# Optimization experiments

Measured on AMD Instinct MI355X. Metric: run time of the kernel, lower is better.

Reference implementation:

```python
import jax, jax.numpy as jnp
import numpy as np

HIDDEN = 1024
HEADS = 16
HEAD_DIM = HIDDEN // HEADS
B, S = 2, 2048


def setup_inputs() -> dict:
    key = jax.random.key(0)
    ks = jax.random.split(key, 9)
    sc = 1.0 / np.sqrt(HIDDEN)
    return {
        "hidden_state": jax.random.normal(ks[0], (B, S, HIDDEN), dtype=jnp.float32),
        "wq": jax.random.normal(ks[1], (HIDDEN, HIDDEN), dtype=jnp.float32) * sc,
        "bq": jax.random.normal(ks[2], (HIDDEN,), dtype=jnp.float32) * 0.01,
        "wk": jax.random.normal(ks[3], (HIDDEN, HIDDEN), dtype=jnp.float32) * sc,
        "bk": jax.random.normal(ks[4], (HIDDEN,), dtype=jnp.float32) * 0.01,
        "wv": jax.random.normal(ks[5], (HIDDEN, HIDDEN), dtype=jnp.float32) * sc,
        "bv": jax.random.normal(ks[6], (HIDDEN,), dtype=jnp.float32) * 0.01,
        "wo": jax.random.normal(ks[7], (HIDDEN, HIDDEN), dtype=jnp.float32) * sc,
        "bo": jax.random.normal(ks[8], (HIDDEN,), dtype=jnp.float32) * 0.01,
    }


def reference(hidden_state, wq, bq, wk, bk, wv, bv, wo, bo):
    b, s, _ = hidden_state.shape

    def split_head(x):  # [B,S,H*D] -> [B,H,S,D]
        return x.reshape(b, s, HEADS, HEAD_DIM).transpose(0, 2, 1, 3)

    q = split_head(hidden_state @ wq + bq)
    k = split_head(hidden_state @ wk + bk)
    v = split_head(hidden_state @ wv + bv)

    # NOTE: original scales by sqrt(hidden_size), NOT sqrt(head_dim)
    scale = 1.0 / jnp.sqrt(jnp.float32(HIDDEN))
    scores = jnp.einsum("bhqd,bhkd->bhqk", q, k) * scale  # [B,H,S,S]
    probs = jax.nn.softmax(scores, axis=-1)
    out = jnp.einsum("bhqk,bhkd->bhqd", probs, v)  # [B,H,S,D]

    # Faithful to source: transpose(-1,-2) then view (this is the original's
    # layout, which differs from the conventional transpose(1,2) merge)
    out = out.transpose(0, 1, 3, 2).reshape(b, -1, HEADS * HEAD_DIM)
    return out @ wo + bo
```

## Files before the change

### kernel.cpp

```cpp
#include <hip/hip_runtime.h>
#include <stdint.h>


typedef unsigned short u16;
typedef __bf16 bf16x8 __attribute__((ext_vector_type(8)));
typedef u16 u16x8 __attribute__((ext_vector_type(8)));
typedef u16 u16x4 __attribute__((ext_vector_type(4)));
typedef float f32x4 __attribute__((ext_vector_type(4)));

#define DEV static __device__ __forceinline__

DEV bf16x8 as_bf16x8(u16x8 u) { union { u16x8 u; bf16x8 b; } c; c.u = u; return c.b; }
DEV u16 f2bf(float f) {
  uint32_t u = __float_as_uint(f);
  u += 0x7fffu + ((u >> 16) & 1u);
  return (u16)(u >> 16);
}
DEV uint32_t pk_rhu(float a, float b) {
  uint32_t ua = (__float_as_uint(a) + 0x8000u) >> 16;
  uint32_t ub = (__float_as_uint(b) + 0x8000u) & 0xffff0000u;
  return ua | ub;
}

DEV void gll16(const u16* g, u16* lds) {
  __builtin_amdgcn_global_load_lds((const __attribute__((address_space(1))) void*)g,
                                   (__attribute__((address_space(3))) void*)lds,
                                   16, 0, 0);
}

__global__ __launch_bounds__(256) void prep_kernel(
    const float* __restrict__ hid, const float* __restrict__ w0,
    const float* __restrict__ w1, const float* __restrict__ w2,
    const float* __restrict__ w3, u16* __restrict__ Ah,
    u16* __restrict__ Wt) {
  __shared__ __align__(16) float T[64][68];
  int bid = blockIdx.x, t = threadIdx.x;
  if (bid < 2048) {
    int i = (bid * 256 + t) * 8;
    f32x4 a = *(const f32x4*)&hid[i];
    f32x4 b = *(const f32x4*)&hid[i + 4];
    u16x8 o;
#pragma unroll
    for (int j = 0; j < 4; ++j) { o[j] = f2bf(a[j]); o[j + 4] = f2bf(b[j]); }
    *(u16x8*)&Ah[i] = o;
    return;
  }
  int tb = bid - 2048;
  int z = tb >> 8, rem = tb & 255;
  const float* W = (z == 0) ? w0 : (z == 1) ? w1 : (z == 2) ? w2 : w3;
  u16* O = Wt + (size_t)z * 1024 * 1024;
  int r0 = (rem >> 4) * 64, c0 = (rem & 15) * 64;
  int i = t >> 2, js = (t & 3) * 16;
#pragma unroll
  for (int jj = 0; jj < 16; jj += 4)
    *(f32x4*)&T[i][js + jj] = *(const f32x4*)&W[(size_t)(r0 + i) * 1024 + c0 + js + jj];
  __syncthreads();
#pragma unroll
  for (int seg = 0; seg < 2; ++seg) {
    u16x8 v;
#pragma unroll
    for (int jj = 0; jj < 8; ++jj) v[jj] = f2bf(T[js + seg * 8 + jj][i]);
    *(u16x8*)&O[(size_t)(c0 + i) * 1024 + r0 + js + seg * 8] = v;
  }
}

DEV void gemm_body(const u16* __restrict__ A, const u16* __restrict__ Bt,
                   const float* __restrict__ bias, u16* __restrict__ C,
                   int mode, float scale) {
  __shared__ __align__(16) u16 As[128 * 32], Bs[128 * 32];
  int tid = threadIdx.x, lane = tid & 63, w = tid >> 6;
  int quad = lane >> 4, l15 = lane & 15;
  int m0 = blockIdx.x * 128, n0 = blockIdx.y * 128;
  int wm = w >> 1, wn = w & 1;
  f32x4 acc[4][4] = {};

  for (int k0 = 0; k0 < 1024; k0 += 32) {
    __syncthreads();
#pragma unroll
    for (int i = 0; i < 2; ++i) {
      int idx = i * 256 + w * 64 + lane;
      int row = idx >> 2, cs = idx & 3, c = cs ^ ((row >> 1) & 3);
      gll16(A + (size_t)(m0 + row) * 1024 + k0 + c * 8, &As[(i * 256 + w * 64) * 8]);
      gll16(Bt + (size_t)(n0 + row) * 1024 + k0 + c * 8, &Bs[(i * 256 + w * 64) * 8]);
    }
    __syncthreads();
    bf16x8 af[4], bfr[4];
#pragma unroll
    for (int mt = 0; mt < 4; ++mt) {
      int row = wm * 64 + mt * 16 + l15;
      af[mt] = as_bf16x8(*(const u16x8*)&As[row * 32 + (quad ^ ((row >> 1) & 3)) * 8]);
    }
#pragma unroll
    for (int nt = 0; nt < 4; ++nt) {
      int row = wn * 64 + nt * 16 + l15;
      bfr[nt] = as_bf16x8(*(const u16x8*)&Bs[row * 32 + (quad ^ ((row >> 1) & 3)) * 8]);
    }
#pragma unroll
    for (int mt = 0; mt < 4; ++mt)
#pragma unroll
      for (int nt = 0; nt < 4; ++nt)
        acc[mt][nt] = __builtin_amdgcn_mfma_f32_16x16x32_bf16(af[mt], bfr[nt], acc[mt][nt], 0, 0, 0);
  }

#pragma unroll
  for (int nt = 0; nt < 4; ++nt) {
    int n = n0 + wn * 64 + nt * 16 + l15;
    float bv = bias[n];
#pragma unroll
    for (int mt = 0; mt < 4; ++mt) {
      int mbase = m0 + wm * 64 + mt * 16 + quad * 4;
      if (mode == 2) {
        int b = mbase >> 11, s = mbase & 2047, h = n >> 6, d = n & 63;
        size_t base = (((size_t)(b * 16 + h)) * 64 + d) * 2048 + s;
        u16x4 pk;
#pragma unroll
        for (int r = 0; r < 4; ++r) pk[r] = f2bf((acc[mt][nt][r] + bv) * scale);
        *(u16x4*)&C[base] = pk;
      } else {
#pragma unroll
        for (int r = 0; r < 4; ++r) {
          int m = mbase + r;
          int b = m >> 11, s = m & 2047, h = n >> 6, d = n & 63;
          C[(((size_t)(b * 16 + h)) * 2048 + s) * 64 + d] =
              f2bf((acc[mt][nt][r] + bv) * scale);
        }
      }
    }
  }
}

__global__ __launch_bounds__(256) void qkv_gemm(
    const u16* __restrict__ A, const u16* __restrict__ Wt,
    const float* __restrict__ bq, const float* __restrict__ bk,
    const float* __restrict__ bv, u16* __restrict__ Qb, u16* __restrict__ Kb,
    u16* __restrict__ Vt) {
  int z = blockIdx.z;
  const u16* Bt = Wt + (size_t)z * 1024 * 1024;
  const float* bias = (z == 0) ? bq : (z == 1) ? bk : bv;
  u16* C = (z == 0) ? Qb : (z == 1) ? Kb : Vt;
  gemm_body(A, Bt, bias, C, (z == 2) ? 2 : 1, (z == 0) ? 0.03125f : 1.0f);
}

__global__ __launch_bounds__(256) void out_gemm(
    const u16* __restrict__ A, const u16* __restrict__ Wt,
    const float* __restrict__ bo, float* __restrict__ C) {
  const u16* Bt = Wt + (size_t)3 * 1024 * 1024;
  __shared__ __align__(16) u16 As[64 * 32], Bs[128 * 32];
  int tid = threadIdx.x, lane = tid & 63, w = tid >> 6;
  int quad = lane >> 4, l15 = lane & 15;
  int m0 = blockIdx.x * 64, n0 = blockIdx.y * 128;
  f32x4 acc[4][2] = {};

  for (int k0 = 0; k0 < 1024; k0 += 32) {
    __syncthreads();
    {
      int idx = w * 64 + lane;
      int row = idx >> 2, cs = idx & 3, c = cs ^ ((row >> 1) & 3);
      gll16(A + (size_t)(m0 + row) * 1024 + k0 + c * 8, &As[(w * 64) * 8]);
#pragma unroll
      for (int i = 0; i < 2; ++i) {
        int bidx = i * 256 + w * 64 + lane;
        int brow = bidx >> 2, bcs = bidx & 3, bc = bcs ^ ((brow >> 1) & 3);
        gll16(Bt + (size_t)(n0 + brow) * 1024 + k0 + bc * 8,
              &Bs[(i * 256 + w * 64) * 8]);
      }
    }
    __syncthreads();
    bf16x8 af[4], bfr[2];
#pragma unroll
    for (int mt = 0; mt < 4; ++mt) {
      int row = mt * 16 + l15;
      af[mt] = as_bf16x8(*(const u16x8*)&As[row * 32 + (quad ^ ((row >> 1) & 3)) * 8]);
    }
#pragma unroll
    for (int nt = 0; nt < 2; ++nt) {
      int row = w * 32 + nt * 16 + l15;
      bfr[nt] = as_bf16x8(*(const u16x8*)&Bs[row * 32 + (quad ^ ((row >> 1) & 3)) * 8]);
    }
#pragma unroll
    for (int mt = 0; mt < 4; ++mt)
#pragma unroll
      for (int nt = 0; nt < 2; ++nt)
        acc[mt][nt] = __builtin_amdgcn_mfma_f32_16x16x32_bf16(af[mt], bfr[nt], acc[mt][nt], 0, 0, 0);
  }

#pragma unroll
  for (int nt = 0; nt < 2; ++nt) {
    int n = n0 + w * 32 + nt * 16 + l15;
    float bv = bo[n];
#pragma unroll
    for (int mt = 0; mt < 4; ++mt) {
      int mbase = m0 + mt * 16 + quad * 4;
#pragma unroll
      for (int r = 0; r < 4; ++r)
        C[(size_t)(mbase + r) * 1024 + n] = acc[mt][nt][r] + bv;
    }
  }
}

#define PSTR 72
__global__ __launch_bounds__(256, 4) void attn_kernel(
    const u16* __restrict__ Qb, const u16* __restrict__ Kb,
    const u16* __restrict__ Vtb, u16* __restrict__ Otb) {
  __shared__ __align__(16) u16 Ks[64 * PSTR], Vs[64 * PSTR];
  __shared__ __align__(16) u16 Pl[4][16 * PSTR];
  int tid = threadIdx.x, lane = tid & 63, w = tid >> 6;
  int quad = lane >> 4, l15 = lane & 15;
  int bh = blockIdx.y, q0 = blockIdx.x * 64;
  const size_t baseQK = (size_t)bh * 2048 * 64;

  int qrow = q0 + w * 16 + l15;
  bf16x8 bq0 = as_bf16x8(*(const u16x8*)&Qb[baseQK + (size_t)qrow * 64 + quad * 8]);
  bf16x8 bq1 = as_bf16x8(*(const u16x8*)&Qb[baseQK + (size_t)qrow * 64 + (4 + quad) * 8]);

  f32x4 o[4] = {};
  float l_run = 0.0f;
  u16* pw = Pl[w];

  u16x8 tk[2], tv[2];
#pragma unroll
  for (int i = 0; i < 2; ++i) {
    int idx = i * 256 + tid;
    int row = idx >> 3, cs = idx & 7;
    tk[i] = *(const u16x8*)&Kb[baseQK + (size_t)row * 64 + cs * 8];
    tv[i] = *(const u16x8*)&Vtb[baseQK + (size_t)row * 2048 + cs * 8];
  }

  for (int kv = 0; kv < 32; ++kv) {
    __syncthreads();
#pragma unroll
    for (int i = 0; i < 2; ++i) {
      int idx = i * 256 + tid;
      int row = idx >> 3, cs = idx & 7;
      *(u16x8*)&Ks[row * PSTR + cs * 8] = tk[i];
      *(u16x8*)&Vs[row * PSTR + cs * 8] = tv[i];
    }
    __syncthreads();

    if (kv < 31) {
#pragma unroll
      for (int i = 0; i < 2; ++i) {
        int idx = i * 256 + tid;
        int row = idx >> 3, cs = idx & 7;
        tk[i] = *(const u16x8*)&Kb[baseQK + (size_t)((kv + 1) * 64 + row) * 64 + cs * 8];
        tv[i] = *(const u16x8*)&Vtb[baseQK + (size_t)row * 2048 + (kv + 1) * 64 + cs * 8];
      }
    }

    f32x4 sc[4] = {};
#pragma unroll
    for (int ks = 0; ks < 2; ++ks) {
      bf16x8 bq = ks ? bq1 : bq0;
#pragma unroll
      for (int mt = 0; mt < 4; ++mt) {
        bf16x8 ak = as_bf16x8(*(const u16x8*)&Ks[(mt * 16 + l15) * PSTR + (ks * 4 + quad) * 8]);
        sc[mt] = __builtin_amdgcn_mfma_f32_16x16x32_bf16(ak, bq, sc[mt], 0, 0, 0);
      }
    }

    float p[4][4];
#pragma unroll
    for (int mt = 0; mt < 4; ++mt)
#pragma unroll
      for (int r = 0; r < 4; ++r) p[mt][r] = __expf(sc[mt][r] - 8.0f);
    float rs = ((p[0][0] + p[0][1]) + (p[0][2] + p[0][3])) +
               ((p[1][0] + p[1][1]) + (p[1][2] + p[1][3])) +
               ((p[2][0] + p[2][1]) + (p[2][2] + p[2][3])) +
               ((p[3][0] + p[3][1]) + (p[3][2] + p[3][3]));
    rs += __shfl_xor(rs, 16, 64);
    rs += __shfl_xor(rs, 32, 64);
    l_run += rs;

#pragma unroll
    for (int mt = 0; mt < 4; ++mt) {
      union { uint32_t u[2]; u16x4 v; } pk;
      pk.u[0] = pk_rhu(p[mt][0], p[mt][1]);
      pk.u[1] = pk_rhu(p[mt][2], p[mt][3]);
      *(u16x4*)&pw[l15 * PSTR + mt * 16 + quad * 4] = pk.v;
    }

#pragma unroll
    for (int ks = 0; ks < 2; ++ks) {
      bf16x8 bp = as_bf16x8(*(const u16x8*)&pw[l15 * PSTR + (ks * 4 + quad) * 8]);
#pragma unroll
      for (int dt = 0; dt < 4; ++dt) {
        bf16x8 av = as_bf16x8(*(const u16x8*)&Vs[(dt * 16 + l15) * PSTR + (ks * 4 + quad) * 8]);
        o[dt] = __builtin_amdgcn_mfma_f32_16x16x32_bf16(av, bp, o[dt], 0, 0, 0);
      }
    }
  }

  float inv = 1.0f / l_run;
#pragma unroll
  for (int dt = 0; dt < 4; ++dt)
#pragma unroll
    for (int r = 0; r < 4; ++r) {
      int d = dt * 16 + quad * 4 + r;
      Otb[(size_t)bh * 64 * 2048 + (size_t)d * 2048 + q0 + w * 16 + l15] =
          f2bf(o[dt][r] * inv);
    }
}

extern "C" void kernel_launch(void* const* d_in, const int* in_sizes, int n_in,
                              void* d_out, int out_size, void* d_ws, size_t ws_size,
                              hipStream_t stream) {
  const float* hid = (const float*)d_in[0];
  const float* wq = (const float*)d_in[1];
  const float* bq = (const float*)d_in[2];
  const float* wk = (const float*)d_in[3];
  const float* bk = (const float*)d_in[4];
  const float* wv = (const float*)d_in[5];
  const float* bv = (const float*)d_in[6];
  const float* wo = (const float*)d_in[7];
  const float* bo = (const float*)d_in[8];

  u16* ws = (u16*)d_ws;
  const size_t MB2 = (size_t)1024 * 1024;
  u16* Wt  = ws;
  u16* Ah  = ws + 4 * MB2;
  u16* Qb  = ws + 8 * MB2;
  u16* Kb  = ws + 12 * MB2;
  u16* Vtb = ws + 16 * MB2;
  u16* Otb = Ah;

  prep_kernel<<<3072, 256, 0, stream>>>(hid, wq, wk, wv, wo, Ah, Wt);
  qkv_gemm<<<dim3(32, 8, 3), 256, 0, stream>>>(Ah, Wt, bq, bk, bv, Qb, Kb, Vtb);
  attn_kernel<<<dim3(32, 32), 256, 0, stream>>>(Qb, Kb, Vtb, Otb);
  out_gemm<<<dim3(64, 8), 256, 0, stream>>>(Otb, Wt, bo, (float*)d_out);
}
```

Baseline: 207.2 us.

## Double attention query rows per wave and deepen QKV GEMM K-tile to 64

Each attention wave now handles two 16-row query groups (128 queries per block), so every K and V fragment read from LDS feeds two MFMAs and the K/V tiles are loaded half as many times overall. The grid shrinks to 512 blocks and launch bounds drop to 2 blocks per SM to make room for the extra registers. Separately, the QKV GEMM K-step grows from 32 to 64 with a wider XOR swizzle, halving the number of barrier pairs per tile. The cost is fewer resident blocks per CU and fewer attention blocks to spread across CUs.

```diff
diff --git a/kernel.cpp b/kernel.cpp
--- a/kernel.cpp
+++ b/kernel.cpp
@@ -67,39 +67,42 @@
 DEV void gemm_body(const u16* __restrict__ A, const u16* __restrict__ Bt,
                    const float* __restrict__ bias, u16* __restrict__ C,
                    int mode, float scale) {
-  __shared__ __align__(16) u16 As[128 * 32], Bs[128 * 32];
+  __shared__ __align__(16) u16 As[128 * 64], Bs[128 * 64];
   int tid = threadIdx.x, lane = tid & 63, w = tid >> 6;
   int quad = lane >> 4, l15 = lane & 15;
   int m0 = blockIdx.x * 128, n0 = blockIdx.y * 128;
   int wm = w >> 1, wn = w & 1;
   f32x4 acc[4][4] = {};
 
-  for (int k0 = 0; k0 < 1024; k0 += 32) {
-    __syncthreads();
-#pragma unroll
-    for (int i = 0; i < 2; ++i) {
+  for (int k0 = 0; k0 < 1024; k0 += 64) {
+    __syncthreads();
+#pragma unroll
+    for (int i = 0; i < 4; ++i) {
       int idx = i * 256 + w * 64 + lane;
-      int row = idx >> 2, cs = idx & 3, c = cs ^ ((row >> 1) & 3);
+      int row = idx >> 3, cs = idx & 7, c = cs ^ (row & 7);
       gll16(A + (size_t)(m0 + row) * 1024 + k0 + c * 8, &As[(i * 256 + w * 64) * 8]);
       gll16(Bt + (size_t)(n0 + row) * 1024 + k0 + c * 8, &Bs[(i * 256 + w * 64) * 8]);
     }
     __syncthreads();
-    bf16x8 af[4], bfr[4];
-#pragma unroll
-    for (int mt = 0; mt < 4; ++mt) {
-      int row = wm * 64 + mt * 16 + l15;
-      af[mt] = as_bf16x8(*(const u16x8*)&As[row * 32 + (quad ^ ((row >> 1) & 3)) * 8]);
-    }
-#pragma unroll
-    for (int nt = 0; nt < 4; ++nt) {
-      int row = wn * 64 + nt * 16 + l15;
-      bfr[nt] = as_bf16x8(*(const u16x8*)&Bs[row * 32 + (quad ^ ((row >> 1) & 3)) * 8]);
-    }
-#pragma unroll
-    for (int mt = 0; mt < 4; ++mt)
-#pragma unroll
-      for (int nt = 0; nt < 4; ++nt)
-        acc[mt][nt] = __builtin_amdgcn_mfma_f32_16x16x32_bf16(af[mt], bfr[nt], acc[mt][nt], 0, 0, 0);
+#pragma unroll
+    for (int s = 0; s < 2; ++s) {
+      bf16x8 af[4], bfr[4];
+#pragma unroll
+      for (int mt = 0; mt < 4; ++mt) {
+        int row = wm * 64 + mt * 16 + l15;
+        af[mt] = as_bf16x8(*(const u16x8*)&As[row * 64 + (((s * 4 + quad) ^ (row & 7)) * 8)]);
+      }
+#pragma unroll
+      for (int nt = 0; nt < 4; ++nt) {
+        int row = wn * 64 + nt * 16 + l15;
+        bfr[nt] = as_bf16x8(*(const u16x8*)&Bs[row * 64 + (((s * 4 + quad) ^ (row & 7)) * 8)]);
+      }
+#pragma unroll
+      for (int mt = 0; mt < 4; ++mt)
+#pragma unroll
+        for (int nt = 0; nt < 4; ++nt)
+          acc[mt][nt] = __builtin_amdgcn_mfma_f32_16x16x32_bf16(af[mt], bfr[nt], acc[mt][nt], 0, 0, 0);
+    }
   }
 
 #pragma unroll
@@ -199,22 +202,27 @@
 }
 
 #define PSTR 72
-__global__ __launch_bounds__(256, 4) void attn_kernel(
+__global__ __launch_bounds__(256, 2) void attn_kernel(
     const u16* __restrict__ Qb, const u16* __restrict__ Kb,
     const u16* __restrict__ Vtb, u16* __restrict__ Otb) {
   __shared__ __align__(16) u16 Ks[64 * PSTR], Vs[64 * PSTR];
-  __shared__ __align__(16) u16 Pl[4][16 * PSTR];
+  __shared__ __align__(16) u16 Pl[4][32 * PSTR];
   int tid = threadIdx.x, lane = tid & 63, w = tid >> 6;
   int quad = lane >> 4, l15 = lane & 15;
-  int bh = blockIdx.y, q0 = blockIdx.x * 64;
+  int bh = blockIdx.y, q0 = blockIdx.x * 128;
   const size_t baseQK = (size_t)bh * 2048 * 64;
 
-  int qrow = q0 + w * 16 + l15;
-  bf16x8 bq0 = as_bf16x8(*(const u16x8*)&Qb[baseQK + (size_t)qrow * 64 + quad * 8]);
-  bf16x8 bq1 = as_bf16x8(*(const u16x8*)&Qb[baseQK + (size_t)qrow * 64 + (4 + quad) * 8]);
-
-  f32x4 o[4] = {};
-  float l_run = 0.0f;
+  bf16x8 bq[2][2];
+#pragma unroll
+  for (int g = 0; g < 2; ++g) {
+    int qrow = q0 + w * 32 + g * 16 + l15;
+#pragma unroll
+    for (int ks = 0; ks < 2; ++ks)
+      bq[g][ks] = as_bf16x8(*(const u16x8*)&Qb[baseQK + (size_t)qrow * 64 + (ks * 4 + quad) * 8]);
+  }
+
+  f32x4 o[2][4] = {};
+  float l_run[2] = {0.0f, 0.0f};
   u16* pw = Pl[w];
 
   u16x8 tk[2], tv[2];
@@ -247,58 +255,68 @@
       }
     }
 
-    f32x4 sc[4] = {};
-#pragma unroll
-    for (int ks = 0; ks < 2; ++ks) {
-      bf16x8 bq = ks ? bq1 : bq0;
+    f32x4 sc[2][4] = {};
+#pragma unroll
+    for (int ks = 0; ks < 2; ++ks)
 #pragma unroll
       for (int mt = 0; mt < 4; ++mt) {
         bf16x8 ak = as_bf16x8(*(const u16x8*)&Ks[(mt * 16 + l15) * PSTR + (ks * 4 + quad) * 8]);
-        sc[mt] = __builtin_amdgcn_mfma_f32_16x16x32_bf16(ak, bq, sc[mt], 0, 0, 0);
-      }
-    }
-
-    float p[4][4];
-#pragma unroll
-    for (int mt = 0; mt < 4; ++mt)
-#pragma unroll
-      for (int r = 0; r < 4; ++r) p[mt][r] = __expf(sc[mt][r] - 8.0f);
-    float rs = ((p[0][0] + p[0][1]) + (p[0][2] + p[0][3])) +
-               ((p[1][0] + p[1][1]) + (p[1][2] + p[1][3])) +
-               ((p[2][0] + p[2][1]) + (p[2][2] + p[2][3])) +
-               ((p[3][0] + p[3][1]) + (p[3][2] + p[3][3]));
-    rs += __shfl_xor(rs, 16, 64);
-    rs += __shfl_xor(rs, 32, 64);
-    l_run += rs;
-
-#pragma unroll
-    for (int mt = 0; mt < 4; ++mt) {
-      union { uint32_t u[2]; u16x4 v; } pk;
-      pk.u[0] = pk_rhu(p[mt][0], p[mt][1]);
-      pk.u[1] = pk_rhu(p[mt][2], p[mt][3]);
-      *(u16x4*)&pw[l15 * PSTR + mt * 16 + quad * 4] = pk.v;
+#pragma unroll
+        for (int g = 0; g < 2; ++g)
+          sc[g][mt] = __builtin_amdgcn_mfma_f32_16x16x32_bf16(ak, bq[g][ks], sc[g][mt], 0, 0, 0);
+      }
+
+#pragma unroll
+    for (int g = 0; g < 2; ++g) {
+      float p[4][4];
+#pragma unroll
+      for (int mt = 0; mt < 4; ++mt)
+#pragma unroll
+        for (int r = 0; r < 4; ++r) p[mt][r] = __expf(sc[g][mt][r] - 8.0f);
+      float rs = ((p[0][0] + p[0][1]) + (p[0][2] + p[0][3])) +
+                 ((p[1][0] + p[1][1]) + (p[1][2] + p[1][3])) +
+                 ((p[2][0] + p[2][1]) + (p[2][2] + p[2][3])) +
+                 ((p[3][0] + p[3][1]) + (p[3][2] + p[3][3]));
+      rs += __shfl_xor(rs, 16, 64);
+      rs += __shfl_xor(rs, 32, 64);
+      l_run[g] += rs;
+#pragma unroll
+      for (int mt = 0; mt < 4; ++mt) {
+        union { uint32_t u[2]; u16x4 v; } pk;
+        pk.u[0] = pk_rhu(p[mt][0], p[mt][1]);
+        pk.u[1] = pk_rhu(p[mt][2], p[mt][3]);
+        *(u16x4*)&pw[(g * 16 + l15) * PSTR + mt * 16 + quad * 4] = pk.v;
+      }
     }
 
 #pragma unroll
     for (int ks = 0; ks < 2; ++ks) {
-      bf16x8 bp = as_bf16x8(*(const u16x8*)&pw[l15 * PSTR + (ks * 4 + quad) * 8]);
+      bf16x8 bp[2];
+#pragma unroll
+      for (int g = 0; g < 2; ++g)
+        bp[g] = as_bf16x8(*(const u16x8*)&pw[(g * 16 + l15) * PSTR + (ks * 4 + quad) * 8]);
 #pragma unroll
       for (int dt = 0; dt < 4; ++dt) {
         bf16x8 av = as_bf16x8(*(const u16x8*)&Vs[(dt * 16 + l15) * PSTR + (ks * 4 + quad) * 8]);
-        o[dt] = __builtin_amdgcn_mfma_f32_16x16x32_bf16(av, bp, o[dt], 0, 0, 0);
-      }
-    }
-  }
-
-  float inv = 1.0f / l_run;
-#pragma unroll
-  for (int dt = 0; dt < 4; ++dt)
-#pragma unroll
-    for (int r = 0; r < 4; ++r) {
-      int d = dt * 16 + quad * 4 + r;
-      Otb[(size_t)bh * 64 * 2048 + (size_t)d * 2048 + q0 + w * 16 + l15] =
-          f2bf(o[dt][r] * inv);
-    }
+#pragma unroll
+        for (int g = 0; g < 2; ++g)
+          o[g][dt] = __builtin_amdgcn_mfma_f32_16x16x32_bf16(av, bp[g], o[g][dt], 0, 0, 0);
+      }
+    }
+  }
+
+#pragma unroll
+  for (int g = 0; g < 2; ++g) {
+    float inv = 1.0f / l_run[g];
+#pragma unroll
+    for (int dt = 0; dt < 4; ++dt)
+#pragma unroll
+      for (int r = 0; r < 4; ++r) {
+        int d = dt * 16 + quad * 4 + r;
+        Otb[(size_t)bh * 64 * 2048 + (size_t)d * 2048 + q0 + w * 32 + g * 16 + l15] =
+            f2bf(o[g][dt][r] * inv);
+      }
+  }
 }
 
 extern "C" void kernel_launch(void* const* d_in, const int* in_sizes, int n_in,
@@ -325,6 +343,6 @@
 
   prep_kernel<<<3072, 256, 0, stream>>>(hid, wq, wk, wv, wo, Ah, Wt);
   qkv_gemm<<<dim3(32, 8, 3), 256, 0, stream>>>(Ah, Wt, bq, bk, bv, Qb, Kb, Vtb);
-  attn_kernel<<<dim3(32, 32), 256, 0, stream>>>(Qb, Kb, Vtb, Otb);
+  attn_kernel<<<dim3(16, 32), 256, 0, stream>>>(Qb, Kb, Vtb, Otb);
   out_gemm<<<dim3(64, 8), 256, 0, stream>>>(Otb, Wt, bo, (float*)d_out);
 }
```

New measurement: 208.5 us. Within noise of the previous version (+0.6%).
